# Kernel optimization log

Hardware: AMD Instinct MI355X
Metric: run time of the kernel (lower is better)

Reference implementation:

```python
import jax, jax.numpy as jnp
import numpy as np

N = 1024   # num proposals
L = 4      # M_score_list_len == len(dy_filter_list)
C = 256    # in_channels
F = 64     # feat_channels
H = 7
W = 7
HW = H * W
OUT = 256  # out_channels


def _ln(x, g, b, eps=1e-5):
    m = jnp.mean(x, axis=-1, keepdims=True)
    v = jnp.mean((x - m) ** 2, axis=-1, keepdims=True)
    return (x - m) * jax.lax.rsqrt(v + eps) * g + b


def setup_inputs() -> dict:
    key = jax.random.key(0)
    ks = jax.random.split(key, 16)

    def w(k, shape, s=0.02):
        return jax.random.normal(k, shape, dtype=jnp.float32) * s

    return {
        "param_feature": jax.random.normal(ks[0], (N, C), dtype=jnp.float32),
        "input_feature": jax.random.normal(ks[1], (N, C, HW), dtype=jnp.float32),
        "pre_in_stack": jax.random.normal(ks[2], (L, N, C, F), dtype=jnp.float32),
        "pre_out_stack": jax.random.normal(ks[3], (L, N, F, OUT), dtype=jnp.float32),
        "W_dyn": w(ks[4], (C, C * F + F * OUT)),
        "b_dyn": jnp.zeros((C * F + F * OUT,), jnp.float32),
        "g_in": jnp.ones((F,), jnp.float32),
        "b_in": jnp.zeros((F,), jnp.float32),
        "g_out": jnp.ones((OUT,), jnp.float32),
        "b_out": jnp.zeros((OUT,), jnp.float32),
        "W_fc": w(ks[5], (OUT * HW, OUT)),
        "b_fc": jnp.zeros((OUT,), jnp.float32),
        "g_fcn": jnp.ones((OUT,), jnp.float32),
        "b_fcn": jnp.zeros((OUT,), jnp.float32),
        "W_M1": w(ks[6], (C, F * L)),
        "b_M1": jnp.zeros((F * L,), jnp.float32),
        "W_M2": w(ks[7], (C, C * L)),
        "b_M2": jnp.zeros((C * L,), jnp.float32),
        "W_S1": w(ks[8], (C, F * L)),
        "b_S1": jnp.zeros((F * L,), jnp.float32),
        "W_S2": w(ks[9], (C, OUT * L)),
        "b_S2": jnp.zeros((OUT * L,), jnp.float32),
        "W_sh": w(ks[10], (H * OUT, H * OUT)),
        "b_sh": jnp.zeros((H * OUT,), jnp.float32),
        "W_sw": w(ks[11], (W * OUT, W * OUT)),
        "b_sw": jnp.zeros((W * OUT,), jnp.float32),
    }


def reference(param_feature, input_feature, pre_in_stack, pre_out_stack,
              W_dyn, b_dyn, g_in, b_in, g_out, b_out,
              W_fc, b_fc, g_fcn, b_fcn,
              W_M1, b_M1, W_M2, b_M2, W_S1, b_S1, W_S2, b_S2,
              W_sh, b_sh, W_sw, b_sw):
    # [N, C, HW] -> [N, HW, C]
    x = jnp.transpose(input_feature.reshape(N, C, HW), (0, 2, 1))

    params = param_feature @ W_dyn + b_dyn
    p_in = params[:, : C * F].reshape(N, C, F)          # [N, C, F]
    p_out = params[:, C * F:].reshape(N, F, OUT)        # [N, F, OUT]

    ori = x
    f = jax.nn.relu(_ln(jnp.einsum('nhc,ncf->nhf', x, p_in), g_in, b_in))
    f = jax.nn.relu(_ln(jnp.einsum('nhf,nfo->nho', f, p_out), g_out, b_out))

    M1 = jax.nn.sigmoid(param_feature @ W_M1 + b_M1).reshape(N, 1, F, L)
    M2 = jax.nn.sigmoid(param_feature @ W_M2 + b_M2).reshape(N, C, 1, L)
    S1 = jax.nn.sigmoid(param_feature @ W_S1 + b_S1).reshape(N, F, 1, L)
    S2 = jax.nn.sigmoid(param_feature @ W_S2 + b_S2).reshape(N, 1, OUT, L)

    for i in range(L):
        m1, m2 = M1[..., i], M2[..., i]
        s1, s2 = S1[..., i], S2[..., i]
        u_in = m1 * pre_in_stack[i] + (1.0 - m1) * p_in
        u_in = m2 * u_in + (1.0 - m2) * p_in
        u_out = s1 * pre_out_stack[i] + (1.0 - s1) * p_out
        u_out = s2 * u_out + (1.0 - s2) * p_out

        fg = f.reshape(N, H, W, OUT)
        fw = (fg.reshape(N, H, W * OUT) @ W_sw + b_sw).reshape(N, HW, OUT)
        fh = (jnp.transpose(fg, (0, 2, 1, 3)).reshape(N, W, H * OUT) @ W_sh + b_sh)
        fh = jnp.transpose(fh.reshape(N, W, H, OUT), (0, 2, 1, 3)).reshape(N, HW, OUT)
        f = fw + fh + ori
        ori = f

        f = jax.nn.relu(_ln(jnp.einsum('nhc,ncf->nhf', x, u_in), g_in, b_in))
        f = jax.nn.relu(_ln(jnp.einsum('nhf,nfo->nho', f, u_out), g_out, b_out))

    f = f.reshape(N, HW * OUT)
    f = jax.nn.relu(_ln(f @ W_fc + b_fc, g_fcn, b_fcn))
    return (f, p_in, p_out)
```

## Files before the change

kernel.cpp:

```cpp
#include <hip/hip_runtime.h>
#include <cstdint>
#include <cstddef>


typedef __attribute__((ext_vector_type(8))) short bf16x8;
typedef __attribute__((ext_vector_type(4))) float floatx4;

#define NPROP 1024
#define CIN   256
#define FEAT  64
#define HWs   49
#define OUTC  256
#define CF    16384
#define KDYN  32768
#define KFC   12544

__device__ __forceinline__ unsigned short f2bfu(float x) {
  union { float f; uint32_t u; } v; v.f = x;
  uint32_t r = v.u + 0x7fffu + ((v.u >> 16) & 1u);
  return (unsigned short)(r >> 16);
}

__global__ __launch_bounds__(256) void k_wdynt(
    const float* __restrict__ W, unsigned short* __restrict__ Bt)
{
  __shared__ float tile[64][65];
  const int k0 = blockIdx.x*64;
  const int o0 = blockIdx.y*64;
  const int t = threadIdx.x;
  const int a = t & 63, b = t >> 6;
  #pragma unroll
  for (int r = 0; r < 16; ++r) {
    const int k = b + (r << 2);
    tile[k][a] = W[(size_t)(k0 + k)*KDYN + o0 + a];
  }
  __syncthreads();
  #pragma unroll
  for (int r = 0; r < 16; ++r) {
    const int o = b + (r << 2);
    Bt[(size_t)(o0 + o)*CIN + k0 + a] = f2bfu(tile[a][o]);
  }
}

__global__ __launch_bounds__(256) void k_abf(
    const float* __restrict__ A, unsigned short* __restrict__ Ab)
{
  const int i = (blockIdx.x*256 + threadIdx.x)*4;
  const float4 v = *(const float4*)(A + i);
  uint2 pk;
  pk.x = (uint32_t)f2bfu(v.x) | ((uint32_t)f2bfu(v.y) << 16);
  pk.y = (uint32_t)f2bfu(v.z) | ((uint32_t)f2bfu(v.w) << 16);
  *(uint2*)(Ab + i) = pk;
}

__global__ __launch_bounds__(256) void k_wgc(
    const float* __restrict__ WM1, const float* __restrict__ WM2,
    const float* __restrict__ WS1, const float* __restrict__ WS2,
    float* __restrict__ Wc)
{
  const int c = blockIdx.x;
  for (int u = threadIdx.x; u < 640; u += 256) {
    const float* W; int col, stride;
    if (u < 64)       { W = WM1; col = u*4 + 3;        stride = 256;  }
    else if (u < 320) { W = WM2; col = (u-64)*4 + 3;   stride = 1024; }
    else if (u < 384) { W = WS1; col = (u-320)*4 + 3;  stride = 256;  }
    else              { W = WS2; col = (u-384)*4 + 3;  stride = 1024; }
    Wc[(size_t)c*640 + u] = W[(size_t)c*stride + col];
  }
}

__global__ __launch_bounds__(256) void k_gates(
    const float* __restrict__ pf, const float* __restrict__ Wc,
    const float* __restrict__ bM1, const float* __restrict__ bM2,
    const float* __restrict__ bS1, const float* __restrict__ bS2,
    float* __restrict__ gm1, float* __restrict__ gm2,
    float* __restrict__ gs1, float* __restrict__ gs2)
{
  const int n = blockIdx.x;
  const int t = threadIdx.x;
  __shared__ float p[CIN];
  p[t] = pf[n*CIN + t];
  __syncthreads();
  for (int u = t; u < 640; u += 256) {
    float acc; float* dst; int idx;
    if (u < 64)       { acc = bM1[u*4 + 3];        dst = gm1 + n*FEAT; idx = u;     }
    else if (u < 320) { acc = bM2[(u-64)*4 + 3];   dst = gm2 + n*CIN;  idx = u-64;  }
    else if (u < 384) { acc = bS1[(u-320)*4 + 3];  dst = gs1 + n*FEAT; idx = u-320; }
    else              { acc = bS2[(u-384)*4 + 3];  dst = gs2 + n*OUTC; idx = u-384; }
    #pragma unroll 8
    for (int c = 0; c < CIN; ++c) acc += p[c] * Wc[(size_t)c*640 + u];
    dst[idx] = 1.0f / (1.0f + __expf(-acc));
  }
}

__global__ __launch_bounds__(256) void k_dyn(
    const unsigned short* __restrict__ Abf, const unsigned short* __restrict__ Bt,
    const float* __restrict__ bias, float* __restrict__ out)
{
  const int bn = blockIdx.x;
  const int bm = blockIdx.y;
  __shared__ short As[128*72];
  __shared__ short Bs[128*72];
  const int t = threadIdx.x;
  const int wave = t >> 6, lane = t & 63;
  const int q = lane >> 4, l15 = lane & 15;
  const int wm = wave >> 1, wn = wave & 1;
  floatx4 acc[4][4];
  #pragma unroll
  for (int mt=0;mt<4;++mt)
    #pragma unroll
    for (int nt=0;nt<4;++nt)
      #pragma unroll
      for (int r=0;r<4;++r) acc[mt][nt][r] = 0.f;

  const int r0 = t >> 3;
  const int kc = (t & 7) * 8;

  for (int ks = 0; ks < 4; ++ks) {
    #pragma unroll
    for (int p = 0; p < 4; ++p) {
      const int row = r0 + p*32;
      *(uint4*)&As[row*72 + kc] =
          *(const uint4*)(Abf + (size_t)(bm*128 + row)*CIN + ks*64 + kc);
      *(uint4*)&Bs[row*72 + kc] =
          *(const uint4*)(Bt  + (size_t)(bn*128 + row)*CIN + ks*64 + kc);
    }
    __syncthreads();
    #pragma unroll
    for (int kk = 0; kk < 2; ++kk) {
      bf16x8 af[4], bfr[4];
      #pragma unroll
      for (int mt = 0; mt < 4; ++mt)
        af[mt] = *(const bf16x8*)&As[(wm*64 + mt*16 + l15)*72 + kk*32 + q*8];
      #pragma unroll
      for (int nt = 0; nt < 4; ++nt)
        bfr[nt] = *(const bf16x8*)&Bs[(wn*64 + nt*16 + l15)*72 + kk*32 + q*8];
      #pragma unroll
      for (int mt = 0; mt < 4; ++mt)
        #pragma unroll
        for (int nt = 0; nt < 4; ++nt)
          acc[mt][nt] = __builtin_amdgcn_mfma_f32_16x16x32_bf16(af[mt], bfr[nt], acc[mt][nt], 0, 0, 0);
    }
    __syncthreads();
  }
  #pragma unroll
  for (int nt = 0; nt < 4; ++nt) {
    const int j = bn*128 + wn*64 + nt*16 + l15;
    const float bv = bias[j];
    float* base; int jj;
    if (j < CF) { base = out + 262144;            jj = j;      }
    else        { base = out + 262144 + 16777216; jj = j - CF; }
    #pragma unroll
    for (int mt = 0; mt < 4; ++mt) {
      const int m0 = bm*128 + wm*64 + mt*16 + q*4;
      #pragma unroll
      for (int r = 0; r < 4; ++r)
        base[(size_t)(m0 + r)*CF + jj] = acc[mt][nt][r] + bv;
    }
  }
}

__global__ __launch_bounds__(256) void k_in(
    const float* __restrict__ infeat, const float* __restrict__ pre3,
    const float* __restrict__ pin,
    const float* __restrict__ gm1, const float* __restrict__ gm2,
    const float* __restrict__ gin, const float* __restrict__ bin,
    float* __restrict__ tbuf)
{
  const int n = blockIdx.x;
  const int t = threadIdx.x;
  const int wave = t >> 6, lane = t & 63;
  __shared__ float us[128*64];
  __shared__ float xs[128*52 + 16];
  __shared__ float m1s[64];
  __shared__ float m2s[256];
  if (t < 64) m1s[t] = gm1[n*64 + t];
  m2s[t] = gm2[n*256 + t];

  float acc[16];
  #pragma unroll
  for (int i = 0; i < 16; ++i) acc[i] = 0.f;

  for (int cc = 0; cc < 2; ++cc) {
    __syncthreads();
    for (int i = t; i < 128*49; i += 256) {
      const int c = i / 49, h = i - c*49;
      xs[c*52 + h] = infeat[(size_t)n*12544 + (size_t)(cc*128 + c)*49 + h];
    }
    for (int i = t*4; i < 8192; i += 1024) {
      const int gi = cc*8192 + i;
      const float4 pr = *(const float4*)(pre3 + (size_t)n*16384 + gi);
      const float4 pp = *(const float4*)(pin  + (size_t)n*16384 + gi);
      const int c = gi >> 6, f0 = gi & 63;
      const float m2v = m2s[c];
      float4 w;
      { const float m1v = m1s[f0+0]; const float ui = m1v*pr.x + (1.f-m1v)*pp.x; w.x = m2v*ui + (1.f-m2v)*pp.x; }
      { const float m1v = m1s[f0+1]; const float ui = m1v*pr.y + (1.f-m1v)*pp.y; w.y = m2v*ui + (1.f-m2v)*pp.y; }
      { const float m1v = m1s[f0+2]; const float ui = m1v*pr.z + (1.f-m1v)*pp.z; w.z = m2v*ui + (1.f-m2v)*pp.z; }
      { const float m1v = m1s[f0+3]; const float ui = m1v*pr.w + (1.f-m1v)*pp.w; w.w = m2v*ui + (1.f-m2v)*pp.w; }
      *(float4*)&us[i] = w;
    }
    __syncthreads();
    #pragma unroll
    for (int p = 0; p < 2; ++p) {
      const int hbase = p*32 + wave*8;
      float* accp = &acc[p*8];
      for (int c = 0; c < 128; ++c) {
        const float uv = us[c*64 + lane];
        const float4 xa = *(const float4*)&xs[c*52 + hbase];
        const float4 xb = *(const float4*)&xs[c*52 + hbase + 4];
        accp[0] += uv*xa.x; accp[1] += uv*xa.y; accp[2] += uv*xa.z; accp[3] += uv*xa.w;
        accp[4] += uv*xb.x; accp[5] += uv*xb.y; accp[6] += uv*xb.z; accp[7] += uv*xb.w;
      }
    }
  }
  const float gv = gin[lane], bv = bin[lane];
  #pragma unroll
  for (int p = 0; p < 2; ++p) {
    const int hbase = p*32 + wave*8;
    #pragma unroll
    for (int j = 0; j < 8; ++j) {
      const int h = hbase + j;
      if (h >= 49) break;
      const float v = acc[p*8+j];
      float s1 = v, s2 = v*v;
      #pragma unroll
      for (int off = 32; off > 0; off >>= 1) {
        s1 += __shfl_xor(s1, off);
        s2 += __shfl_xor(s2, off);
      }
      const float mean = s1 * (1.f/64.f);
      const float var  = s2 * (1.f/64.f) - mean*mean;
      const float rs   = rsqrtf(var + 1e-5f);
      const float o    = (v - mean)*rs*gv + bv;
      tbuf[(size_t)(n*49 + h)*64 + lane] = fmaxf(o, 0.f);
    }
  }
}

__global__ __launch_bounds__(256) void k_out(
    const float* __restrict__ tbuf, const float* __restrict__ pre3,
    const float* __restrict__ pout,
    const float* __restrict__ gs1, const float* __restrict__ gs2,
    const float* __restrict__ gout, const float* __restrict__ bout,
    unsigned short* __restrict__ fbuf)
{
  const int n = blockIdx.x;
  const int t = threadIdx.x;
  const int wave = t >> 6, lane = t & 63;
  __shared__ float u2s[32*256];
  __shared__ float ts2[64*52 + 16];
  __shared__ float s1s[64];
  __shared__ float s2s[256];
  if (t < 64) s1s[t] = gs1[n*64 + t];
  s2s[t] = gs2[n*256 + t];
  for (int i = t; i < 3136; i += 256) {
    const int h = i >> 6, f = i & 63;
    ts2[f*52 + h] = tbuf[(size_t)n*3136 + i];
  }

  float acc[2][8][4];
  #pragma unroll
  for (int p=0;p<2;++p)
    #pragma unroll
    for (int j=0;j<8;++j)
      #pragma unroll
      for (int k=0;k<4;++k) acc[p][j][k] = 0.f;

  for (int fc_ = 0; fc_ < 2; ++fc_) {
    __syncthreads();
    for (int i = t*4; i < 8192; i += 1024) {
      const int gi = fc_*8192 + i;
      const float4 pr = *(const float4*)(pre3 + (size_t)n*16384 + gi);
      const float4 pp = *(const float4*)(pout + (size_t)n*16384 + gi);
      const int f = gi >> 8, o0 = gi & 255;
      const float s1v = s1s[f];
      float4 w;
      { const float s2v = s2s[o0+0]; const float uo = s1v*pr.x + (1.f-s1v)*pp.x; w.x = s2v*uo + (1.f-s2v)*pp.x; }
      { const float s2v = s2s[o0+1]; const float uo = s1v*pr.y + (1.f-s1v)*pp.y; w.y = s2v*uo + (1.f-s2v)*pp.y; }
      { const float s2v = s2s[o0+2]; const float uo = s1v*pr.z + (1.f-s1v)*pp.z; w.z = s2v*uo + (1.f-s2v)*pp.z; }
      { const float s2v = s2s[o0+3]; const float uo = s1v*pr.w + (1.f-s1v)*pp.w; w.w = s2v*uo + (1.f-s2v)*pp.w; }
      *(float4*)&u2s[i] = w;
    }
    __syncthreads();
    #pragma unroll
    for (int p = 0; p < 2; ++p) {
      const int hbase = (p*4 + wave)*8;
      for (int fl = 0; fl < 32; ++fl) {
        const float u0 = u2s[fl*256 + lane];
        const float u1 = u2s[fl*256 + lane + 64];
        const float u2v= u2s[fl*256 + lane + 128];
        const float u3 = u2s[fl*256 + lane + 192];
        const int f = fc_*32 + fl;
        const float4 ta = *(const float4*)&ts2[f*52 + hbase];
        const float4 tb = *(const float4*)&ts2[f*52 + hbase + 4];
        const float tv[8] = {ta.x,ta.y,ta.z,ta.w,tb.x,tb.y,tb.z,tb.w};
        #pragma unroll
        for (int j = 0; j < 8; ++j) {
          acc[p][j][0] += tv[j]*u0;
          acc[p][j][1] += tv[j]*u1;
          acc[p][j][2] += tv[j]*u2v;
          acc[p][j][3] += tv[j]*u3;
        }
      }
    }
  }
  const float go0=gout[lane], go1=gout[lane+64], go2=gout[lane+128], go3=gout[lane+192];
  const float bo0=bout[lane], bo1=bout[lane+64], bo2=bout[lane+128], bo3=bout[lane+192];
  #pragma unroll
  for (int p = 0; p < 2; ++p) {
    const int hbase = (p*4 + wave)*8;
    #pragma unroll
    for (int j = 0; j < 8; ++j) {
      const int h = hbase + j;
      if (h >= 49) break;
      const float v0 = acc[p][j][0], v1 = acc[p][j][1], v2 = acc[p][j][2], v3 = acc[p][j][3];
      float s1 = v0+v1+v2+v3;
      float s2 = v0*v0+v1*v1+v2*v2+v3*v3;
      #pragma unroll
      for (int off = 32; off > 0; off >>= 1) {
        s1 += __shfl_xor(s1, off);
        s2 += __shfl_xor(s2, off);
      }
      const float mean = s1 * (1.f/256.f);
      const float var  = s2 * (1.f/256.f) - mean*mean;
      const float rs   = rsqrtf(var + 1e-5f);
      unsigned short* dst = fbuf + (size_t)(n*49 + h)*256;
      dst[lane      ] = f2bfu(fmaxf((v0-mean)*rs*go0 + bo0, 0.f));
      dst[lane + 64 ] = f2bfu(fmaxf((v1-mean)*rs*go1 + bo1, 0.f));
      dst[lane + 128] = f2bfu(fmaxf((v2-mean)*rs*go2 + bo2, 0.f));
      dst[lane + 192] = f2bfu(fmaxf((v3-mean)*rs*go3 + bo3, 0.f));
    }
  }
}

__global__ __launch_bounds__(256) void k_wfct(
    const float* __restrict__ W, unsigned short* __restrict__ Wt)
{
  __shared__ float tile[64][65];
  const int k0 = blockIdx.x*64, o0 = blockIdx.y*64;
  const int t = threadIdx.x;
  const int a = t & 63, b = t >> 6;
  #pragma unroll
  for (int r = 0; r < 16; ++r) {
    const int k = b + (r << 2);
    tile[k][a] = W[(size_t)(k0 + k)*256 + o0 + a];
  }
  __syncthreads();
  #pragma unroll
  for (int r = 0; r < 16; ++r) {
    const int o = b + (r << 2);
    Wt[(size_t)(o0 + o)*KFC + k0 + a] = f2bfu(tile[a][o]);
  }
}

__global__ __launch_bounds__(256) void k_fc(
    const unsigned short* __restrict__ Abf, const unsigned short* __restrict__ Bbf,
    float* __restrict__ part)
{
  const int bm = blockIdx.x, bn = blockIdx.y, bk = blockIdx.z;
  __shared__ short As[64*72];
  __shared__ short Bs[128*72];
  const int t = threadIdx.x;
  const int wave = t >> 6, lane = t & 63;
  const int q = lane >> 4, l15 = lane & 15;
  floatx4 acc[4][2];
  #pragma unroll
  for (int mt=0;mt<4;++mt)
    #pragma unroll
    for (int nt=0;nt<2;++nt)
      #pragma unroll
      for (int r=0;r<4;++r) acc[mt][nt][r] = 0.f;

  for (int ks = 0; ks < 14; ++ks) {
    const int k0 = bk*896 + ks*64;
    {
      int row = t >> 3; const int kc = (t & 7) * 8;
      #pragma unroll
      for (int p2 = 0; p2 < 2; ++p2, row += 32) {
        const uint4 v = *(const uint4*)(Abf + (size_t)(bm*64 + row)*KFC + k0 + kc);
        *(uint4*)&As[row*72 + kc] = v;
      }
    }
    {
      int col = t >> 3; const int kc = (t & 7) * 8;
      #pragma unroll
      for (int p2 = 0; p2 < 4; ++p2, col += 32) {
        const uint4 v = *(const uint4*)(Bbf + (size_t)(bn*128 + col)*KFC + k0 + kc);
        *(uint4*)&Bs[col*72 + kc] = v;
      }
    }
    __syncthreads();
    #pragma unroll
    for (int kk = 0; kk < 2; ++kk) {
      bf16x8 af[4], bfr[2];
      #pragma unroll
      for (int mt = 0; mt < 4; ++mt)
        af[mt] = *(const bf16x8*)&As[(mt*16 + l15)*72 + kk*32 + q*8];
      #pragma unroll
      for (int nt = 0; nt < 2; ++nt)
        bfr[nt] = *(const bf16x8*)&Bs[(wave*32 + nt*16 + l15)*72 + kk*32 + q*8];
      #pragma unroll
      for (int mt = 0; mt < 4; ++mt)
        #pragma unroll
        for (int nt = 0; nt < 2; ++nt)
          acc[mt][nt] = __builtin_amdgcn_mfma_f32_16x16x32_bf16(af[mt], bfr[nt], acc[mt][nt], 0, 0, 0);
    }
    __syncthreads();
  }
  float* dst = part + (size_t)bk*NPROP*OUTC;
  #pragma unroll
  for (int mt = 0; mt < 4; ++mt)
    #pragma unroll
    for (int nt = 0; nt < 2; ++nt) {
      const int o  = bn*128 + wave*32 + nt*16 + l15;
      const int m0 = bm*64 + mt*16 + q*4;
      #pragma unroll
      for (int r = 0; r < 4; ++r)
        dst[(size_t)(m0 + r)*OUTC + o] = acc[mt][nt][r];
    }
}

__global__ __launch_bounds__(256) void k_fcred(
    const float* __restrict__ part, const float* __restrict__ bfc,
    const float* __restrict__ gn, const float* __restrict__ bnm,
    float* __restrict__ out0)
{
  const int n = blockIdx.x, t = threadIdx.x;
  float acc = bfc[t];
  #pragma unroll
  for (int s = 0; s < 14; ++s) acc += part[(size_t)s*NPROP*OUTC + n*256 + t];
  __shared__ float red[8];
  float s1 = acc, s2 = acc*acc;
  #pragma unroll
  for (int off = 32; off > 0; off >>= 1) {
    s1 += __shfl_xor(s1, off);
    s2 += __shfl_xor(s2, off);
  }
  const int wave = t >> 6, lane = t & 63;
  if (lane == 0) { red[wave] = s1; red[4+wave] = s2; }
  __syncthreads();
  const float S1 = red[0]+red[1]+red[2]+red[3];
  const float S2 = red[4]+red[5]+red[6]+red[7];
  const float mean = S1 * (1.f/256.f);
  const float var  = S2 * (1.f/256.f) - mean*mean;
  const float rs   = rsqrtf(var + 1e-5f);
  const float v = (acc - mean)*rs*gn[t] + bnm[t];
  out0[n*256 + t] = fmaxf(v, 0.f);
}

extern "C" void kernel_launch(void* const* d_in, const int* in_sizes, int n_in,
                              void* d_out, int out_size, void* d_ws, size_t ws_size,
                              hipStream_t stream)
{
  const float* pf    = (const float*)d_in[0];
  const float* infe  = (const float*)d_in[1];
  const float* preI  = (const float*)d_in[2];
  const float* preO  = (const float*)d_in[3];
  const float* Wdyn  = (const float*)d_in[4];
  const float* bdyn  = (const float*)d_in[5];
  const float* g_in  = (const float*)d_in[6];
  const float* b_in  = (const float*)d_in[7];
  const float* g_out = (const float*)d_in[8];
  const float* b_out = (const float*)d_in[9];
  const float* Wfc   = (const float*)d_in[10];
  const float* bfc   = (const float*)d_in[11];
  const float* gfcn  = (const float*)d_in[12];
  const float* bfcn  = (const float*)d_in[13];
  const float* WM1   = (const float*)d_in[14];
  const float* bM1   = (const float*)d_in[15];
  const float* WM2   = (const float*)d_in[16];
  const float* bM2   = (const float*)d_in[17];
  const float* WS1   = (const float*)d_in[18];
  const float* bS1   = (const float*)d_in[19];
  const float* WS2   = (const float*)d_in[20];
  const float* bS2   = (const float*)d_in[21];

  char* wsb = (char*)d_ws;
  float* gm1  = (float*)(wsb + 0);
  float* gm2  = (float*)(wsb + 262144);
  float* gs1  = (float*)(wsb + 1310720);
  float* gs2  = (float*)(wsb + 1572864);
  unsigned short* wdynt = (unsigned short*)(wsb + 2621440);
  float* tbuf = (float*)(wsb + 2621440);
  float* part = (float*)(wsb + 2621440);
  unsigned short* fbuf = (unsigned short*)(wsb + 19398656);
  unsigned short* abf  = (unsigned short*)(wsb + 19398656);
  float* wgc           = (float*)(wsb + 19398656 + 524288);
  unsigned short* wfct = (unsigned short*)(wsb + 45088768);

  const float* pre_in3  = preI + (size_t)3*NPROP*CIN*FEAT;
  const float* pre_out3 = preO + (size_t)3*NPROP*FEAT*OUTC;
  const float* p_in  = (const float*)d_out + 262144;
  const float* p_out = (const float*)d_out + 262144 + 16777216;
  float* out0 = (float*)d_out;

  k_wdynt<<<dim3(4, 512), 256, 0, stream>>>(Wdyn, wdynt);
  k_abf  <<<dim3(256),    256, 0, stream>>>(pf, abf);
  k_wgc  <<<dim3(256),    256, 0, stream>>>(WM1, WM2, WS1, WS2, wgc);
  k_wfct <<<dim3(196, 4), 256, 0, stream>>>(Wfc, wfct);
  k_gates<<<dim3(1024),   256, 0, stream>>>(pf, wgc, bM1, bM2, bS1, bS2,
                                            gm1, gm2, gs1, gs2);
  k_dyn  <<<dim3(256, 8), 256, 0, stream>>>(abf, wdynt, bdyn, (float*)d_out);
  k_in   <<<dim3(1024),   256, 0, stream>>>(infe, pre_in3, p_in, gm1, gm2, g_in, b_in, tbuf);
  k_out  <<<dim3(1024),   256, 0, stream>>>(tbuf, pre_out3, p_out, gs1, gs2, g_out, b_out, fbuf);
  k_fc   <<<dim3(16, 2, 14), 256, 0, stream>>>(fbuf, wfct, part);
  k_fcred<<<dim3(1024),   256, 0, stream>>>(part, bfc, gfcn, bfcn, out0);
}
```

Measured before the change: 815.7 us.

## Merge prep kernels, compute gates via MFMA GEMM, fuse in/out stages

Four weight/activation preparation kernels are merged into one launch. The gate computation becomes a bf16 MFMA GEMM with the sigmoid applied in the epilogue, replacing the scalar per-proposal loop. The input and output dynamic-conv stages are fused into one kernel that keeps the intermediate in shared memory instead of writing it to a global tbuf. This cuts launch count and global traffic, but the gates now run in bf16 and the fused kernel uses more shared memory per block, which may lower occupancy.

Measured after the change: 781.1 us. -4.2%, faster.

```diff
diff --git a/kernel.cpp b/kernel.cpp
--- a/kernel.cpp
+++ b/kernel.cpp
@@ -21,81 +21,72 @@
   return (unsigned short)(r >> 16);
 }
 
-__global__ __launch_bounds__(256) void k_wdynt(
-    const float* __restrict__ W, unsigned short* __restrict__ Bt)
-{
-  __shared__ float tile[64][65];
-  const int k0 = blockIdx.x*64;
-  const int o0 = blockIdx.y*64;
-  const int t = threadIdx.x;
-  const int a = t & 63, b = t >> 6;
-  #pragma unroll
-  for (int r = 0; r < 16; ++r) {
-    const int k = b + (r << 2);
-    tile[k][a] = W[(size_t)(k0 + k)*KDYN + o0 + a];
-  }
-  __syncthreads();
-  #pragma unroll
-  for (int r = 0; r < 16; ++r) {
-    const int o = b + (r << 2);
-    Bt[(size_t)(o0 + o)*CIN + k0 + a] = f2bfu(tile[a][o]);
-  }
-}
-
-__global__ __launch_bounds__(256) void k_abf(
-    const float* __restrict__ A, unsigned short* __restrict__ Ab)
-{
-  const int i = (blockIdx.x*256 + threadIdx.x)*4;
-  const float4 v = *(const float4*)(A + i);
-  uint2 pk;
-  pk.x = (uint32_t)f2bfu(v.x) | ((uint32_t)f2bfu(v.y) << 16);
-  pk.y = (uint32_t)f2bfu(v.z) | ((uint32_t)f2bfu(v.w) << 16);
-  *(uint2*)(Ab + i) = pk;
-}
-
-__global__ __launch_bounds__(256) void k_wgc(
+__global__ __launch_bounds__(256) void k_prep(
+    const float* __restrict__ Wdyn, unsigned short* __restrict__ wdynt,
+    const float* __restrict__ Wfc,  unsigned short* __restrict__ wfct,
+    const float* __restrict__ pf,   unsigned short* __restrict__ abf,
     const float* __restrict__ WM1, const float* __restrict__ WM2,
     const float* __restrict__ WS1, const float* __restrict__ WS2,
-    float* __restrict__ Wc)
-{
-  const int c = blockIdx.x;
-  for (int u = threadIdx.x; u < 640; u += 256) {
-    const float* W; int col, stride;
-    if (u < 64)       { W = WM1; col = u*4 + 3;        stride = 256;  }
-    else if (u < 320) { W = WM2; col = (u-64)*4 + 3;   stride = 1024; }
-    else if (u < 384) { W = WS1; col = (u-320)*4 + 3;  stride = 256;  }
-    else              { W = WS2; col = (u-384)*4 + 3;  stride = 1024; }
-    Wc[(size_t)c*640 + u] = W[(size_t)c*stride + col];
-  }
-}
-
-__global__ __launch_bounds__(256) void k_gates(
-    const float* __restrict__ pf, const float* __restrict__ Wc,
     const float* __restrict__ bM1, const float* __restrict__ bM2,
     const float* __restrict__ bS1, const float* __restrict__ bS2,
+    unsigned short* __restrict__ wgcb, float* __restrict__ bgc)
+{
+  __shared__ float tile[64][65];
+  const int b = blockIdx.x;
+  const int t = threadIdx.x;
+  if (b < 2048) {
+    const int k0 = (b & 3)*64, o0 = (b >> 2)*64;
+    const int a = t & 63, w = t >> 6;
+    #pragma unroll
+    for (int r = 0; r < 16; ++r) {
+      const int k = w + (r << 2);
+      tile[k][a] = Wdyn[(size_t)(k0 + k)*KDYN + o0 + a];
+    }
+    __syncthreads();
+    #pragma unroll
+    for (int r = 0; r < 16; ++r) {
+      const int o = w + (r << 2);
+      wdynt[(size_t)(o0 + o)*CIN + k0 + a] = f2bfu(tile[a][o]);
+    }
+  } else if (b < 2832) {
+    const int b2 = b - 2048;
+    const int k0 = (b2 % 196)*64, o0 = (b2 / 196)*64;
+    const int a = t & 63, w = t >> 6;
+    #pragma unroll
+    for (int r = 0; r < 16; ++r) {
+      const int k = w + (r << 2);
+      tile[k][a] = Wfc[(size_t)(k0 + k)*256 + o0 + a];
+    }
+    __syncthreads();
+    #pragma unroll
+    for (int r = 0; r < 16; ++r) {
+      const int o = w + (r << 2);
+      wfct[(size_t)(o0 + o)*KFC + k0 + a] = f2bfu(tile[a][o]);
+    }
+  } else if (b < 3088) {
+    const int i = ((b - 2832)*256 + t)*4;
+    const float4 v = *(const float4*)(pf + i);
+    uint2 pk;
+    pk.x = (uint32_t)f2bfu(v.x) | ((uint32_t)f2bfu(v.y) << 16);
+    pk.y = (uint32_t)f2bfu(v.z) | ((uint32_t)f2bfu(v.w) << 16);
+    *(uint2*)(abf + i) = pk;
+  } else {
+    const int u = b - 3088;
+    const float* W; const float* bb; int col, stride;
+    if (u < 64)       { W = WM1; bb = bM1; col = u*4 + 3;        stride = 256;  }
+    else if (u < 320) { W = WM2; bb = bM2; col = (u-64)*4 + 3;   stride = 1024; }
+    else if (u < 384) { W = WS1; bb = bS1; col = (u-320)*4 + 3;  stride = 256;  }
+    else              { W = WS2; bb = bS2; col = (u-384)*4 + 3;  stride = 1024; }
+    wgcb[(size_t)u*256 + t] = f2bfu(W[(size_t)t*stride + col]);
+    if (t == 0) bgc[u] = bb[col];
+  }
+}
+
+__global__ __launch_bounds__(256) void k_gatesM(
+    const unsigned short* __restrict__ Abf, const unsigned short* __restrict__ Wcb,
+    const float* __restrict__ bgc,
     float* __restrict__ gm1, float* __restrict__ gm2,
     float* __restrict__ gs1, float* __restrict__ gs2)
-{
-  const int n = blockIdx.x;
-  const int t = threadIdx.x;
-  __shared__ float p[CIN];
-  p[t] = pf[n*CIN + t];
-  __syncthreads();
-  for (int u = t; u < 640; u += 256) {
-    float acc; float* dst; int idx;
-    if (u < 64)       { acc = bM1[u*4 + 3];        dst = gm1 + n*FEAT; idx = u;     }
-    else if (u < 320) { acc = bM2[(u-64)*4 + 3];   dst = gm2 + n*CIN;  idx = u-64;  }
-    else if (u < 384) { acc = bS1[(u-320)*4 + 3];  dst = gs1 + n*FEAT; idx = u-320; }
-    else              { acc = bS2[(u-384)*4 + 3];  dst = gs2 + n*OUTC; idx = u-384; }
-    #pragma unroll 8
-    for (int c = 0; c < CIN; ++c) acc += p[c] * Wc[(size_t)c*640 + u];
-    dst[idx] = 1.0f / (1.0f + __expf(-acc));
-  }
-}
-
-__global__ __launch_bounds__(256) void k_dyn(
-    const unsigned short* __restrict__ Abf, const unsigned short* __restrict__ Bt,
-    const float* __restrict__ bias, float* __restrict__ out)
 {
   const int bn = blockIdx.x;
   const int bm = blockIdx.y;
@@ -123,6 +114,76 @@
       *(uint4*)&As[row*72 + kc] =
           *(const uint4*)(Abf + (size_t)(bm*128 + row)*CIN + ks*64 + kc);
       *(uint4*)&Bs[row*72 + kc] =
+          *(const uint4*)(Wcb + (size_t)(bn*128 + row)*CIN + ks*64 + kc);
+    }
+    __syncthreads();
+    #pragma unroll
+    for (int kk = 0; kk < 2; ++kk) {
+      bf16x8 af[4], bfr[4];
+      #pragma unroll
+      for (int mt = 0; mt < 4; ++mt)
+        af[mt] = *(const bf16x8*)&As[(wm*64 + mt*16 + l15)*72 + kk*32 + q*8];
+      #pragma unroll
+      for (int nt = 0; nt < 4; ++nt)
+        bfr[nt] = *(const bf16x8*)&Bs[(wn*64 + nt*16 + l15)*72 + kk*32 + q*8];
+      #pragma unroll
+      for (int mt = 0; mt < 4; ++mt)
+        #pragma unroll
+        for (int nt = 0; nt < 4; ++nt)
+          acc[mt][nt] = __builtin_amdgcn_mfma_f32_16x16x32_bf16(af[mt], bfr[nt], acc[mt][nt], 0, 0, 0);
+    }
+    __syncthreads();
+  }
+  #pragma unroll
+  for (int nt = 0; nt < 4; ++nt) {
+    const int j = bn*128 + wn*64 + nt*16 + l15;
+    const float bv = bgc[j];
+    #pragma unroll
+    for (int mt = 0; mt < 4; ++mt) {
+      const int m0 = bm*128 + wm*64 + mt*16 + q*4;
+      #pragma unroll
+      for (int r = 0; r < 4; ++r) {
+        const int n = m0 + r;
+        const float v = 1.0f / (1.0f + __expf(-(acc[mt][nt][r] + bv)));
+        if (j < 64)       gm1[n*FEAT + j]        = v;
+        else if (j < 320) gm2[n*CIN  + (j-64)]   = v;
+        else if (j < 384) gs1[n*FEAT + (j-320)]  = v;
+        else              gs2[n*OUTC + (j-384)]  = v;
+      }
+    }
+  }
+}
+
+__global__ __launch_bounds__(256) void k_dyn(
+    const unsigned short* __restrict__ Abf, const unsigned short* __restrict__ Bt,
+    const float* __restrict__ bias, float* __restrict__ out)
+{
+  const int bn = blockIdx.x;
+  const int bm = blockIdx.y;
+  __shared__ short As[128*72];
+  __shared__ short Bs[128*72];
+  const int t = threadIdx.x;
+  const int wave = t >> 6, lane = t & 63;
+  const int q = lane >> 4, l15 = lane & 15;
+  const int wm = wave >> 1, wn = wave & 1;
+  floatx4 acc[4][4];
+  #pragma unroll
+  for (int mt=0;mt<4;++mt)
+    #pragma unroll
+    for (int nt=0;nt<4;++nt)
+      #pragma unroll
+      for (int r=0;r<4;++r) acc[mt][nt][r] = 0.f;
+
+  const int r0 = t >> 3;
+  const int kc = (t & 7) * 8;
+
+  for (int ks = 0; ks < 4; ++ks) {
+    #pragma unroll
+    for (int p = 0; p < 4; ++p) {
+      const int row = r0 + p*32;
+      *(uint4*)&As[row*72 + kc] =
+          *(const uint4*)(Abf + (size_t)(bm*128 + row)*CIN + ks*64 + kc);
+      *(uint4*)&Bs[row*72 + kc] =
           *(const uint4*)(Bt  + (size_t)(bn*128 + row)*CIN + ks*64 + kc);
     }
     __syncthreads();
@@ -160,119 +221,104 @@
   }
 }
 
-__global__ __launch_bounds__(256) void k_in(
-    const float* __restrict__ infeat, const float* __restrict__ pre3,
-    const float* __restrict__ pin,
+__global__ __launch_bounds__(256) void k_inout(
+    const float* __restrict__ infeat,
+    const float* __restrict__ preI3, const float* __restrict__ pin,
+    const float* __restrict__ preO3, const float* __restrict__ pout,
     const float* __restrict__ gm1, const float* __restrict__ gm2,
+    const float* __restrict__ gs1, const float* __restrict__ gs2,
     const float* __restrict__ gin, const float* __restrict__ bin,
-    float* __restrict__ tbuf)
+    const float* __restrict__ gout, const float* __restrict__ bout,
+    unsigned short* __restrict__ fbuf)
 {
   const int n = blockIdx.x;
   const int t = threadIdx.x;
   const int wave = t >> 6, lane = t & 63;
-  __shared__ float us[128*64];
+  __shared__ float us[8192];
   __shared__ float xs[128*52 + 16];
-  __shared__ float m1s[64];
-  __shared__ float m2s[256];
-  if (t < 64) m1s[t] = gm1[n*64 + t];
+  __shared__ float ts2[64*52 + 16];
+  __shared__ float m1s[64], s1s[64];
+  __shared__ float m2s[256], s2s[256];
+  if (t < 64) { m1s[t] = gm1[n*64 + t]; s1s[t] = gs1[n*64 + t]; }
   m2s[t] = gm2[n*256 + t];
-
-  float acc[16];
-  #pragma unroll
-  for (int i = 0; i < 16; ++i) acc[i] = 0.f;
-
-  for (int cc = 0; cc < 2; ++cc) {
-    __syncthreads();
-    for (int i = t; i < 128*49; i += 256) {
-      const int c = i / 49, h = i - c*49;
-      xs[c*52 + h] = infeat[(size_t)n*12544 + (size_t)(cc*128 + c)*49 + h];
-    }
-    for (int i = t*4; i < 8192; i += 1024) {
-      const int gi = cc*8192 + i;
-      const float4 pr = *(const float4*)(pre3 + (size_t)n*16384 + gi);
-      const float4 pp = *(const float4*)(pin  + (size_t)n*16384 + gi);
-      const int c = gi >> 6, f0 = gi & 63;
-      const float m2v = m2s[c];
-      float4 w;
-      { const float m1v = m1s[f0+0]; const float ui = m1v*pr.x + (1.f-m1v)*pp.x; w.x = m2v*ui + (1.f-m2v)*pp.x; }
-      { const float m1v = m1s[f0+1]; const float ui = m1v*pr.y + (1.f-m1v)*pp.y; w.y = m2v*ui + (1.f-m2v)*pp.y; }
-      { const float m1v = m1s[f0+2]; const float ui = m1v*pr.z + (1.f-m1v)*pp.z; w.z = m2v*ui + (1.f-m2v)*pp.z; }
-      { const float m1v = m1s[f0+3]; const float ui = m1v*pr.w + (1.f-m1v)*pp.w; w.w = m2v*ui + (1.f-m2v)*pp.w; }
-      *(float4*)&us[i] = w;
-    }
-    __syncthreads();
+  s2s[t] = gs2[n*256 + t];
+
+  {
+    float acc[16];
+    #pragma unroll
+    for (int i = 0; i < 16; ++i) acc[i] = 0.f;
+
+    for (int cc = 0; cc < 2; ++cc) {
+      __syncthreads();
+      for (int i = t; i < 128*49; i += 256) {
+        const int c = i / 49, h = i - c*49;
+        xs[c*52 + h] = infeat[(size_t)n*12544 + (size_t)(cc*128 + c)*49 + h];
+      }
+      for (int i = t*4; i < 8192; i += 1024) {
+        const int gi = cc*8192 + i;
+        const float4 pr = *(const float4*)(preI3 + (size_t)n*16384 + gi);
+        const float4 pp = *(const float4*)(pin   + (size_t)n*16384 + gi);
+        const int c = gi >> 6, f0 = gi & 63;
+        const float m2v = m2s[c];
+        float4 w;
+        { const float m1v = m1s[f0+0]; const float ui = m1v*pr.x + (1.f-m1v)*pp.x; w.x = m2v*ui + (1.f-m2v)*pp.x; }
+        { const float m1v = m1s[f0+1]; const float ui = m1v*pr.y + (1.f-m1v)*pp.y; w.y = m2v*ui + (1.f-m2v)*pp.y; }
+        { const float m1v = m1s[f0+2]; const float ui = m1v*pr.z + (1.f-m1v)*pp.z; w.z = m2v*ui + (1.f-m2v)*pp.z; }
+        { const float m1v = m1s[f0+3]; const float ui = m1v*pr.w + (1.f-m1v)*pp.w; w.w = m2v*ui + (1.f-m2v)*pp.w; }
+        *(float4*)&us[i] = w;
+      }
+      __syncthreads();
+      #pragma unroll
+      for (int p = 0; p < 2; ++p) {
+        const int hbase = p*32 + wave*8;
+        float* accp = &acc[p*8];
+        for (int c = 0; c < 128; ++c) {
+          const float uv = us[c*64 + lane];
+          const float4 xa = *(const float4*)&xs[c*52 + hbase];
+          const float4 xb = *(const float4*)&xs[c*52 + hbase + 4];
+          accp[0] += uv*xa.x; accp[1] += uv*xa.y; accp[2] += uv*xa.z; accp[3] += uv*xa.w;
+          accp[4] += uv*xb.x; accp[5] += uv*xb.y; accp[6] += uv*xb.z; accp[7] += uv*xb.w;
+        }
+      }
+    }
+    const float gv = gin[lane], bv = bin[lane];
     #pragma unroll
     for (int p = 0; p < 2; ++p) {
       const int hbase = p*32 + wave*8;
-      float* accp = &acc[p*8];
-      for (int c = 0; c < 128; ++c) {
-        const float uv = us[c*64 + lane];
-        const float4 xa = *(const float4*)&xs[c*52 + hbase];
-        const float4 xb = *(const float4*)&xs[c*52 + hbase + 4];
-        accp[0] += uv*xa.x; accp[1] += uv*xa.y; accp[2] += uv*xa.z; accp[3] += uv*xa.w;
-        accp[4] += uv*xb.x; accp[5] += uv*xb.y; accp[6] += uv*xb.z; accp[7] += uv*xb.w;
-      }
-    }
-  }
-  const float gv = gin[lane], bv = bin[lane];
-  #pragma unroll
-  for (int p = 0; p < 2; ++p) {
-    const int hbase = p*32 + wave*8;
-    #pragma unroll
-    for (int j = 0; j < 8; ++j) {
-      const int h = hbase + j;
-      if (h >= 49) break;
-      const float v = acc[p*8+j];
-      float s1 = v, s2 = v*v;
-      #pragma unroll
-      for (int off = 32; off > 0; off >>= 1) {
-        s1 += __shfl_xor(s1, off);
-        s2 += __shfl_xor(s2, off);
-      }
-      const float mean = s1 * (1.f/64.f);
-      const float var  = s2 * (1.f/64.f) - mean*mean;
-      const float rs   = rsqrtf(var + 1e-5f);
-      const float o    = (v - mean)*rs*gv + bv;
-      tbuf[(size_t)(n*49 + h)*64 + lane] = fmaxf(o, 0.f);
-    }
-  }
-}
-
-__global__ __launch_bounds__(256) void k_out(
-    const float* __restrict__ tbuf, const float* __restrict__ pre3,
-    const float* __restrict__ pout,
-    const float* __restrict__ gs1, const float* __restrict__ gs2,
-    const float* __restrict__ gout, const float* __restrict__ bout,
-    unsigned short* __restrict__ fbuf)
-{
-  const int n = blockIdx.x;
-  const int t = threadIdx.x;
-  const int wave = t >> 6, lane = t & 63;
-  __shared__ float u2s[32*256];
-  __shared__ float ts2[64*52 + 16];
-  __shared__ float s1s[64];
-  __shared__ float s2s[256];
-  if (t < 64) s1s[t] = gs1[n*64 + t];
-  s2s[t] = gs2[n*256 + t];
-  for (int i = t; i < 3136; i += 256) {
-    const int h = i >> 6, f = i & 63;
-    ts2[f*52 + h] = tbuf[(size_t)n*3136 + i];
-  }
-
-  float acc[2][8][4];
+      #pragma unroll
+      for (int j = 0; j < 8; ++j) {
+        const int h = hbase + j;
+        if (h >= 49) break;
+        const float v = acc[p*8+j];
+        float s1 = v, s2 = v*v;
+        #pragma unroll
+        for (int off = 32; off > 0; off >>= 1) {
+          s1 += __shfl_xor(s1, off);
+          s2 += __shfl_xor(s2, off);
+        }
+        const float mean = s1 * (1.f/64.f);
+        const float var  = s2 * (1.f/64.f) - mean*mean;
+        const float rs   = rsqrtf(var + 1e-5f);
+        const float o    = (v - mean)*rs*gv + bv;
+        ts2[lane*52 + h] = fmaxf(o, 0.f);
+      }
+    }
+  }
+
+  float acc2[2][8][4];
   #pragma unroll
   for (int p=0;p<2;++p)
     #pragma unroll
     for (int j=0;j<8;++j)
       #pragma unroll
-      for (int k=0;k<4;++k) acc[p][j][k] = 0.f;
+      for (int k=0;k<4;++k) acc2[p][j][k] = 0.f;
 
   for (int fc_ = 0; fc_ < 2; ++fc_) {
     __syncthreads();
     for (int i = t*4; i < 8192; i += 1024) {
       const int gi = fc_*8192 + i;
-      const float4 pr = *(const float4*)(pre3 + (size_t)n*16384 + gi);
-      const float4 pp = *(const float4*)(pout + (size_t)n*16384 + gi);
+      const float4 pr = *(const float4*)(preO3 + (size_t)n*16384 + gi);
+      const float4 pp = *(const float4*)(pout  + (size_t)n*16384 + gi);
       const int f = gi >> 8, o0 = gi & 255;
       const float s1v = s1s[f];
       float4 w;
@@ -280,27 +326,27 @@
       { const float s2v = s2s[o0+1]; const float uo = s1v*pr.y + (1.f-s1v)*pp.y; w.y = s2v*uo + (1.f-s2v)*pp.y; }
       { const float s2v = s2s[o0+2]; const float uo = s1v*pr.z + (1.f-s1v)*pp.z; w.z = s2v*uo + (1.f-s2v)*pp.z; }
       { const float s2v = s2s[o0+3]; const float uo = s1v*pr.w + (1.f-s1v)*pp.w; w.w = s2v*uo + (1.f-s2v)*pp.w; }
-      *(float4*)&u2s[i] = w;
+      *(float4*)&us[i] = w;
     }
     __syncthreads();
     #pragma unroll
     for (int p = 0; p < 2; ++p) {
       const int hbase = (p*4 + wave)*8;
       for (int fl = 0; fl < 32; ++fl) {
-        const float u0 = u2s[fl*256 + lane];
-        const float u1 = u2s[fl*256 + lane + 64];
-        const float u2v= u2s[fl*256 + lane + 128];
-        const float u3 = u2s[fl*256 + lane + 192];
+        const float u0 = us[fl*256 + lane];
+        const float u1 = us[fl*256 + lane + 64];
+        const float u2v= us[fl*256 + lane + 128];
+        const float u3 = us[fl*256 + lane + 192];
         const int f = fc_*32 + fl;
         const float4 ta = *(const float4*)&ts2[f*52 + hbase];
         const float4 tb = *(const float4*)&ts2[f*52 + hbase + 4];
         const float tv[8] = {ta.x,ta.y,ta.z,ta.w,tb.x,tb.y,tb.z,tb.w};
         #pragma unroll
         for (int j = 0; j < 8; ++j) {
-          acc[p][j][0] += tv[j]*u0;
-          acc[p][j][1] += tv[j]*u1;
-          acc[p][j][2] += tv[j]*u2v;
-          acc[p][j][3] += tv[j]*u3;
+          acc2[p][j][0] += tv[j]*u0;
+          acc2[p][j][1] += tv[j]*u1;
+          acc2[p][j][2] += tv[j]*u2v;
+          acc2[p][j][3] += tv[j]*u3;
         }
       }
     }
@@ -314,7 +360,7 @@
     for (int j = 0; j < 8; ++j) {
       const int h = hbase + j;
       if (h >= 49) break;
-      const float v0 = acc[p][j][0], v1 = acc[p][j][1], v2 = acc[p][j][2], v3 = acc[p][j][3];
+      const float v0 = acc2[p][j][0], v1 = acc2[p][j][1], v2 = acc2[p][j][2], v3 = acc2[p][j][3];
       float s1 = v0+v1+v2+v3;
       float s2 = v0*v0+v1*v1+v2*v2+v3*v3;
       #pragma unroll
@@ -331,26 +377,6 @@
       dst[lane + 128] = f2bfu(fmaxf((v2-mean)*rs*go2 + bo2, 0.f));
       dst[lane + 192] = f2bfu(fmaxf((v3-mean)*rs*go3 + bo3, 0.f));
     }
-  }
-}
-
-__global__ __launch_bounds__(256) void k_wfct(
-    const float* __restrict__ W, unsigned short* __restrict__ Wt)
-{
-  __shared__ float tile[64][65];
-  const int k0 = blockIdx.x*64, o0 = blockIdx.y*64;
-  const int t = threadIdx.x;
-  const int a = t & 63, b = t >> 6;
-  #pragma unroll
-  for (int r = 0; r < 16; ++r) {
-    const int k = b + (r << 2);
-    tile[k][a] = W[(size_t)(k0 + k)*256 + o0 + a];
-  }
-  __syncthreads();
-  #pragma unroll
-  for (int r = 0; r < 16; ++r) {
-    const int o = b + (r << 2);
-    Wt[(size_t)(o0 + o)*KFC + k0 + a] = f2bfu(tile[a][o]);
   }
 }
 
@@ -482,12 +508,12 @@
   float* gs1  = (float*)(wsb + 1310720);
   float* gs2  = (float*)(wsb + 1572864);
   unsigned short* wdynt = (unsigned short*)(wsb + 2621440);
-  float* tbuf = (float*)(wsb + 2621440);
-  float* part = (float*)(wsb + 2621440);
-  unsigned short* fbuf = (unsigned short*)(wsb + 19398656);
-  unsigned short* abf  = (unsigned short*)(wsb + 19398656);
-  float* wgc           = (float*)(wsb + 19398656 + 524288);
-  unsigned short* wfct = (unsigned short*)(wsb + 45088768);
+  unsigned short* wfct  = (unsigned short*)(wsb + 19398656);
+  unsigned short* abf   = (unsigned short*)(wsb + 25821184);
+  unsigned short* wgcb  = (unsigned short*)(wsb + 26345472);
+  float* bgc  = (float*)(wsb + 26673152);
+  float* part = (float*)(wsb + 26677248);
+  unsigned short* fbuf  = (unsigned short*)(wsb + 41357312);
 
   const float* pre_in3  = preI + (size_t)3*NPROP*CIN*FEAT;
   const float* pre_out3 = preO + (size_t)3*NPROP*FEAT*OUTC;
@@ -495,15 +521,14 @@
   const float* p_out = (const float*)d_out + 262144 + 16777216;
   float* out0 = (float*)d_out;
 
-  k_wdynt<<<dim3(4, 512), 256, 0, stream>>>(Wdyn, wdynt);
-  k_abf  <<<dim3(256),    256, 0, stream>>>(pf, abf);
-  k_wgc  <<<dim3(256),    256, 0, stream>>>(WM1, WM2, WS1, WS2, wgc);
-  k_wfct <<<dim3(196, 4), 256, 0, stream>>>(Wfc, wfct);
-  k_gates<<<dim3(1024),   256, 0, stream>>>(pf, wgc, bM1, bM2, bS1, bS2,
-                                            gm1, gm2, gs1, gs2);
-  k_dyn  <<<dim3(256, 8), 256, 0, stream>>>(abf, wdynt, bdyn, (float*)d_out);
-  k_in   <<<dim3(1024),   256, 0, stream>>>(infe, pre_in3, p_in, gm1, gm2, g_in, b_in, tbuf);
-  k_out  <<<dim3(1024),   256, 0, stream>>>(tbuf, pre_out3, p_out, gs1, gs2, g_out, b_out, fbuf);
-  k_fc   <<<dim3(16, 2, 14), 256, 0, stream>>>(fbuf, wfct, part);
-  k_fcred<<<dim3(1024),   256, 0, stream>>>(part, bfc, gfcn, bfcn, out0);
-}
+  k_prep  <<<dim3(3728),     256, 0, stream>>>(Wdyn, wdynt, Wfc, wfct, pf, abf,
+                                               WM1, WM2, WS1, WS2,
+                                               bM1, bM2, bS1, bS2, wgcb, bgc);
+  k_gatesM<<<dim3(5, 8),     256, 0, stream>>>(abf, wgcb, bgc, gm1, gm2, gs1, gs2);
+  k_dyn   <<<dim3(256, 8),   256, 0, stream>>>(abf, wdynt, bdyn, (float*)d_out);
+  k_inout <<<dim3(1024),     256, 0, stream>>>(infe, pre_in3, p_in, pre_out3, p_out,
+                                               gm1, gm2, gs1, gs2,
+                                               g_in, b_in, g_out, b_out, fbuf);
+  k_fc    <<<dim3(16, 2, 14),256, 0, stream>>>(fbuf, wfct, part);
+  k_fcred <<<dim3(1024),     256, 0, stream>>>(part, bfc, gfcn, bfcn, out0);
+}
```
